# Kernel tuning notes

Hardware: AMD Instinct MI355X
Metric: run time of the kernel (lower is better)

## Reference

```python
import jax, jax.numpy as jnp
import numpy as np

B, C, H, W, KS = 8, 3, 512, 512, 3
K = KS * KS  # kernel_elements = 9


def setup_inputs() -> dict:
    key = jax.random.key(0)
    ks = jax.random.split(key, 5)
    return {
        "x": jax.random.normal(ks[0], (B, C, H, W), jnp.float32),
        "w1": jax.random.normal(ks[1], (K - 1, C, KS, KS), jnp.float32) * 0.1,  # find_ref conv weight
        "b1": jax.random.normal(ks[2], (K - 1,), jnp.float32) * 0.1,
        "w2": jax.random.normal(ks[3], (C, K), jnp.float32) * 0.1,  # grouped 1x1 conv: C groups, K in-ch each
        "b2": jax.random.normal(ks[4], (C,), jnp.float32) * 0.1,
    }


def _grid_sample_bilinear(img_nhwc, gx, gy):
    # torch.grid_sample, mode='bilinear', padding_mode='zeros', align_corners=False
    # img_nhwc: [B,H,W,C]; gx,gy: [B,h,w,K] normalized coords (x=width, y=height)
    Bs, Hh, Ww, _ = img_nhwc.shape
    ix = ((gx + 1.0) * Ww - 1.0) * 0.5
    iy = ((gy + 1.0) * Hh - 1.0) * 0.5
    ix0 = jnp.floor(ix)
    iy0 = jnp.floor(iy)
    wx1 = ix - ix0
    wy1 = iy - iy0
    wx0 = 1.0 - wx1
    wy0 = 1.0 - wy1
    bidx = jnp.arange(Bs)[:, None, None, None]

    def corner(yc, xc, wgt):
        valid = (xc >= 0) & (xc < Ww) & (yc >= 0) & (yc < Hh)
        xi = jnp.clip(xc, 0, Ww - 1).astype(jnp.int32)
        yi = jnp.clip(yc, 0, Hh - 1).astype(jnp.int32)
        v = img_nhwc[bidx, yi, xi]  # [B,h,w,K,C]
        return v * (wgt * valid)[..., None]

    out = corner(iy0, ix0, wy0 * wx0)
    out = out + corner(iy0, ix0 + 1.0, wy0 * wx1)
    out = out + corner(iy0 + 1.0, ix0, wy1 * wx0)
    out = out + corner(iy0 + 1.0, ix0 + 1.0, wy1 * wx1)
    return out  # [B,h,w,K,C]


def _forward(x, w1, b1, w2, b2):
    Bs, Cc, Hh, Ww = x.shape
    pad = KS // 2
    # find_ref: conv3x3 (pad=1) + sigmoid -> offsets in [0,1]
    off = jax.lax.conv_general_dilated(
        x, w1, (1, 1), ((pad, pad), (pad, pad)),
        dimension_numbers=("NCHW", "OIHW", "NCHW"))
    off = jax.nn.sigmoid(off + b1[None, :, None, None])  # [B,K-1,H,W]
    off = jnp.transpose(off, (0, 2, 3, 1)).reshape(Bs, Hh, Ww, (K - 1) // 2, 2)
    ctr = float(KS // 2)
    sym = 2.0 * ctr - off  # find_symmetric_points
    center = jnp.zeros((Bs, Hh, Ww, 1, 2), off.dtype)
    off_all = jnp.concatenate([off, center, sym], axis=-2)  # [B,H,W,K,2]
    # base grid: stack(h_grid, w_grid) with linspace(0,1)
    base = jnp.stack(
        jnp.meshgrid(jnp.linspace(0.0, 1.0, Hh), jnp.linspace(0.0, 1.0, Ww), indexing="ij"),
        axis=-1)  # [H,W,2]
    coords = base[None, :, :, None, :] + off_all  # [B,H,W,K,2]
    # grid_sample interprets last dim as (x=width, y=height)
    gx = coords[..., 0]
    gy = coords[..., 1]
    img = jnp.transpose(x, (0, 2, 3, 1))  # [B,H,W,C]
    sampled = _grid_sample_bilinear(img, gx, gy)  # [B,H,W,K,C]
    # concatenation order in torch: elem-major channels -> [B, K*C, H, W]
    deformed = jnp.transpose(sampled, (0, 3, 4, 1, 2)).reshape(Bs, K * Cc, Hh, Ww)
    # grouped 1x1 conv: groups=C, group g consumes channels [g*K:(g+1)*K]
    grp = deformed.reshape(Bs, Cc, K, Hh, Ww)
    out = jnp.einsum("bgkhw,gk->bghw", grp, w2) + b2[None, :, None, None]
    return jax.nn.relu(out)


def reference(x, w1, b1, w2, b2):
    return _forward(x, w1, b1, w2, b2)
```

## Files before the change

### kernel.cpp

```cpp
#include <hip/hip_runtime.h>

#define BATCH 8
#define HDIM  512
#define WDIM  512
#define PLANE (HDIM * WDIM)

#define QN      129
#define QPAIRS  (QN * QN)
#define QPLANE  (4 * QPAIRS * 8)
#define IMG12   (5 * QPLANE)

#define QC_N      129
#define YROW0     254
#define YROWS     259
#define YSTRIDE   260
#define QSTRIDE   (YSTRIDE * 16)
#define PARSTRIDE (QC_N * QSTRIDE)
#define IMGSTRIDE (2 * PARSTRIDE)

typedef _Float16 half2v __attribute__((ext_vector_type(2)));
typedef _Float16 half4v __attribute__((ext_vector_type(4)));
typedef _Float16 half8v __attribute__((ext_vector_type(8)));
typedef float    f2v    __attribute__((ext_vector_type(2)));

struct __align__(16) HQuad { half2v p0, p1, p2, p3; };
struct __align__(8)  HPair { half2v lo, hi; };

#if __has_builtin(__builtin_amdgcn_fdot2)
#define FDOT2(a, b, c) __builtin_amdgcn_fdot2((a), (b), (c), false)
#else
#define FDOT2(a, b, c) fmaf((float)(a).x, (float)(b).x, fmaf((float)(a).y, (float)(b).y, (c)))
#endif

#if __has_builtin(__builtin_amdgcn_exp2f)
#define EXP2F(x) __builtin_amdgcn_exp2f(x)
#else
#define EXP2F(x) exp2f(x)
#endif

__global__ __launch_bounds__(256) void repack_dots(
    const float* __restrict__ x,
    const float* __restrict__ w2,
    char* __restrict__ xp)
{
    int b  = blockIdx.x & 7;
    int P  = (blockIdx.x >> 3) & 3;
    int Qy = blockIdx.x >> 5;
    int Qx = threadIdx.x;
    if (Qx >= QN) return;
    int px = P & 1, py = P >> 1;
    int X0 = 2 * Qx + 254 + px;
    int Y0 = 2 * Qy + 254 + py;

    const float* xb = x + (size_t)b * 3 * PLANE;

    float vc[4][3];
#pragma unroll
    for (int cy = 0; cy < 2; cy++)
#pragma unroll
        for (int cx = 0; cx < 2; cx++) {
            int xx = X0 + cx, yy = Y0 + cy;
            bool vld = (xx <= 511) && (yy <= 511);
            int xs = min(xx, 511), ys = min(yy, 511);
            int base = (ys << 9) + xs;
            int ci = cy * 2 + cx;
            vc[ci][0] = vld ? xb[base]             : 0.f;
            vc[ci][1] = vld ? xb[PLANE + base]     : 0.f;
            vc[ci][2] = vld ? xb[2 * PLANE + base] : 0.f;
        }

    char* dst = xp + (size_t)b * IMG12 + (size_t)((P * QPAIRS + Qy * QN + Qx) << 3);
#pragma unroll
    for (int q = 0; q < 5; q++) {
        float wa = w2[3 * q], wb = w2[3 * q + 1], wc = w2[3 * q + 2];
        half4v o;
#pragma unroll
        for (int ci = 0; ci < 4; ci++) {
            float v = fmaf(vc[ci][2], wc, fmaf(vc[ci][1], wb, vc[ci][0] * wa));
            o[ci] = (_Float16)v;
        }
        *(half4v*)(dst + q * QPLANE) = o;
    }
}

__global__ __launch_bounds__(256) void seesaw_v12(
    const float* __restrict__ x,
    const char* __restrict__ xpack,
    const float* __restrict__ w1, const float* __restrict__ b1,
    const float* __restrict__ w2, const float* __restrict__ b2,
    float* __restrict__ out)
{
    int t  = threadIdx.x;
    int b  = blockIdx.x & 7;
    int i  = blockIdx.x >> 3;
    int j0 = t << 1;

    const float* xb = x + (size_t)b * 3 * PLANE;
    const char*  hb = xpack + (size_t)b * IMG12;

    int cm = j0 - 1; if (cm < 0) cm = 0;
    int cp = j0 + 2; if (cp > 511) cp = 511;
    bool jlo = (t == 0), jhi = (t == 255);

    float vm[9], va[9], vb9[9], vp9[9];
    if (i >= 1 && i <= 510) {
#pragma unroll
        for (int di = 0; di < 3; di++) {
            const float* row = xb + ((i + di - 1) << 9);
#pragma unroll
            for (int c = 0; c < 3; c++) {
                const float* rc = row + c * PLANE;
                float m = rc[cm]; if (jlo) m = 0.f;
                f2v  mid = *(const f2v*)(rc + j0);
                float pv = rc[cp]; if (jhi) pv = 0.f;
                int r = c * 3 + di;
                vm[r] = m; va[r] = mid[0]; vb9[r] = mid[1]; vp9[r] = pv;
            }
        }
    } else {
#pragma unroll
        for (int di = 0; di < 3; di++) {
            int y = i + di - 1;
            bool yv = (unsigned)y < (unsigned)HDIM;
            const float* row = xb + ((yv ? y : 0) << 9);
#pragma unroll
            for (int c = 0; c < 3; c++) {
                const float* rc = row + c * PLANE;
                float m = rc[cm]; if (jlo || !yv) m = 0.f;
                f2v  mid = *(const f2v*)(rc + j0);
                float pv = rc[cp]; if (jhi || !yv) pv = 0.f;
                float m0 = yv ? mid[0] : 0.f;
                float m1 = yv ? mid[1] : 0.f;
                int r = c * 3 + di;
                vm[r] = m; va[r] = m0; vb9[r] = m1; vp9[r] = pv;
            }
        }
    }
    __builtin_amdgcn_sched_barrier(0);

    float tap0[27], tap1[27];
#pragma unroll
    for (int c = 0; c < 3; c++)
#pragma unroll
        for (int di = 0; di < 3; di++) {
            int r = c * 3 + di, k = c * 9 + di * 3;
            tap0[k]     = vm[r];  tap0[k + 1] = va[r];  tap0[k + 2] = vb9[r];
            tap1[k]     = va[r];  tap1[k + 1] = vb9[r]; tap1[k + 2] = vp9[r];
        }

    const float NLOG2E = -1.44269504f;
    auto conv8 = [&](const float* tap, float* s2) {
        f2v V[13];
#pragma unroll
        for (int k = 0; k < 13; k++) { V[k][0] = tap[2 * k]; V[k][1] = tap[2 * k + 1]; }
#pragma unroll
        for (int e = 0; e < 8; e++) {
            const float* we = w1 + e * 27;
            f2v a2; a2[0] = b1[e]; a2[1] = 0.f;
#pragma unroll
            for (int k = 0; k < 13; k++) {
                f2v ww; ww[0] = we[2 * k]; ww[1] = we[2 * k + 1];
                a2 = __builtin_elementwise_fma(V[k], ww, a2);
            }
            float acc = a2[0] + a2[1] + tap[26] * we[26];
            s2[e] = 256.0f * __builtin_amdgcn_rcpf(1.0f + EXP2F(acc * NLOG2E));
        }
    };
    float s0[8], s1[8];
    conv8(tap0, s0);
    conv8(tap1, s1);

    const float k511 = 256.0f / 511.0f;
    float fxb = fmaf((float)i, k511, 255.5f);
    float fy0 = fmaf((float)j0, k511, 255.5f);
    float fy1 = fy0 + k511;

    int   adrA[5], adrB[5];
    float wXA[5][2], wYA[5][2], wXB[5][2], wYB[5][2];
    auto phase1 = [&](const float* s2, float fyb, int (&adr)[5],
                      float (&wX)[5][2], float (&wY)[5][2]) {
#pragma unroll
        for (int q = 0; q < 5; q++) {
            float ixf = (q < 4) ? (fxb + s2[2 * q])     : fxb;
            float iyf = (q < 4) ? (fyb + s2[2 * q + 1]) : fyb;
            int ix0 = (int)ixf, iy0 = (int)iyf;
            float wx1 = ixf - (float)ix0, wy1 = iyf - (float)iy0;
            wX[q][0] = (ix0 <= 511) ? (1.f - wx1) : 0.f;
            wX[q][1] = (ix0 <= 510) ? wx1 : 0.f;
            wY[q][0] = (iy0 <= 511) ? (1.f - wy1) : 0.f;
            wY[q][1] = (iy0 <= 510) ? wy1 : 0.f;
            int x0c = min(ix0, 511), y0c = min(iy0, 511);
            int P  = ((y0c & 1) << 1) | (x0c & 1);
            int Qx = (x0c >> 1) - 127;
            int Qy = (y0c >> 1) - 127;
            adr[q] = (P * QPAIRS + Qy * QN + Qx) << 3;
        }
    };

    phase1(s0, fy0, adrA, wXA, wYA);
    HPair pA[5];
#pragma unroll
    for (int q = 0; q < 5; q++)
        pA[q] = *(const HPair*)(hb + (size_t)(q * QPLANE + adrA[q]));
    phase1(s1, fy1, adrB, wXB, wYB);
    HPair pB[5];
#pragma unroll
    for (int q = 0; q < 5; q++)
        pB[q] = *(const HPair*)(hb + (size_t)(q * QPLANE + adrB[q]));
    __builtin_amdgcn_sched_barrier(0);

    float ogA[3] = {0.f, 0.f, 0.f}, ogB[3] = {0.f, 0.f, 0.f};
    auto phase3 = [&](HPair (&pv)[5], float (&wX)[5][2], float (&wY)[5][2], float* og) {
#pragma unroll
        for (int q = 0; q < 5; q++) {
            int g = q / 3;
            float v00 = (float)pv[q].lo[0], v01 = (float)pv[q].lo[1];
            float v10 = (float)pv[q].hi[0], v11c = (float)pv[q].hi[1];
            float r0 = fmaf(v01,  wX[q][1], v00 * wX[q][0]);
            float r1 = fmaf(v11c, wX[q][1], v10 * wX[q][0]);
            og[g] = fmaf(r1, wY[q][1], fmaf(r0, wY[q][0], og[g]));
        }
    };
    phase3(pA, wXA, wYA, ogA);
    phase3(pB, wXB, wYB, ogB);

    if ((i | j0) == 0) {
#pragma unroll
        for (int p = 5; p < 9; p++) {
            float ixf = fxb + 512.0f - s0[2 * (p - 5)];
            float iyf = fy0 + 512.0f - s0[2 * (p - 5) + 1];
            float ix0f = floorf(ixf), iy0f = floorf(iyf);
            float wx1 = ixf - ix0f, wy1 = iyf - iy0f;
            float wx0 = 1.f - wx1,  wy0 = 1.f - wy1;
            int ix0 = (int)ix0f, iy0 = (int)iy0f;
            float t0 = 0.f, t1 = 0.f, t2 = 0.f;
            for (int cy = 0; cy < 2; cy++) {
                int yc2 = iy0 + cy;
                if (yc2 < 0 || yc2 >= HDIM) continue;
                float wy = cy ? wy1 : wy0;
                for (int cx = 0; cx < 2; cx++) {
                    int xcc2 = ix0 + cx;
                    if (xcc2 < 0 || xcc2 >= WDIM) continue;
                    float wgt = wy * (cx ? wx1 : wx0);
                    int base = (yc2 << 9) + xcc2;
                    t0 = fmaf(xb[base],             wgt, t0);
                    t1 = fmaf(xb[PLANE + base],     wgt, t1);
                    t2 = fmaf(xb[2 * PLANE + base], wgt, t2);
                }
            }
            int g  = p / 3;
            int k0 = (p % 3) * 3;
            ogA[g] = fmaf(t0, w2[g * 9 + k0 + 0], ogA[g]);
            ogA[g] = fmaf(t1, w2[g * 9 + k0 + 1], ogA[g]);
            ogA[g] = fmaf(t2, w2[g * 9 + k0 + 2], ogA[g]);
        }
    }

    size_t ob = (size_t)(b * 3) * PLANE + ((size_t)i << 9) + j0;
#pragma unroll
    for (int g = 0; g < 3; g++) {
        float u0 = ogA[g] + b2[g];
        float u1 = ogB[g] + b2[g];
        f2v st;
        st[0] = u0 > 0.f ? u0 : 0.f;
        st[1] = u1 > 0.f ? u1 : 0.f;
        *(f2v*)(out + ob + (size_t)g * PLANE) = st;
    }
}

__global__ __launch_bounds__(256) void repack_tiles(
    const float* __restrict__ x, char* __restrict__ xp)
{
    int b    = blockIdx.x & 7;
    int rest = blockIdx.x >> 3;
    int p    = rest & 1;
    int Qc   = rest >> 1;
    int xb0  = 254 + 2 * Qc + p;
    int x1   = xb0 + 1;
    bool x1v = (x1 < 512);

    const float* xb = x + (size_t)b * 3 * PLANE;
    char* dst = xp + (size_t)b * IMGSTRIDE + (size_t)p * PARSTRIDE
                   + (size_t)Qc * QSTRIDE;

    for (int t = threadIdx.x; t < YROWS; t += 256) {
        int y = YROW0 + t;
        half8v o;
        if (y < 512) {
            int base = (y << 9) + xb0;
            float a0 = xb[base];
            float a1 = xb[PLANE + base];
            float a2 = xb[2 * PLANE + base];
            float b0 = 0.f, b1c = 0.f, b2c = 0.f;
            if (x1v) {
                b0  = xb[base + 1];
                b1c = xb[PLANE + base + 1];
                b2c = xb[2 * PLANE + base + 1];
            }
            o[0] = (_Float16)a0; o[1] = (_Float16)a1; o[2] = (_Float16)a2; o[3] = (_Float16)0.f;
            o[4] = (_Float16)b0; o[5] = (_Float16)b1c; o[6] = (_Float16)b2c; o[7] = (_Float16)0.f;
        } else {
#pragma unroll
            for (int k = 0; k < 8; k++) o[k] = (_Float16)0.f;
        }
        *(half8v*)(dst + (size_t)t * 16) = o;
    }
}

__global__ __launch_bounds__(256) void seesaw_v11(
    const float* __restrict__ x, const char* __restrict__ xpack,
    const float* __restrict__ w1, const float* __restrict__ b1,
    const float* __restrict__ w2, const float* __restrict__ b2,
    float* __restrict__ out)
{
    int t  = threadIdx.x;
    int b  = blockIdx.x & 7;
    int i  = blockIdx.x >> 3;
    int j0 = t << 1;

    const float* xb = x + (size_t)b * 3 * PLANE;
    const char*  hb = xpack + (size_t)b * IMGSTRIDE;

    int cm = j0 - 1; if (cm < 0) cm = 0;
    int cp = j0 + 2; if (cp > 511) cp = 511;
    bool jlo = (t == 0), jhi = (t == 255);

    float vm[9], va[9], vb9[9], vp9[9];
    if (i >= 1 && i <= 510) {
#pragma unroll
        for (int di = 0; di < 3; di++) {
            const float* row = xb + ((i + di - 1) << 9);
#pragma unroll
            for (int c = 0; c < 3; c++) {
                const float* rc = row + c * PLANE;
                float m = rc[cm]; if (jlo) m = 0.f;
                f2v  mid = *(const f2v*)(rc + j0);
                float pv = rc[cp]; if (jhi) pv = 0.f;
                int r = c * 3 + di;
                vm[r] = m; va[r] = mid[0]; vb9[r] = mid[1]; vp9[r] = pv;
            }
        }
    } else {
#pragma unroll
        for (int di = 0; di < 3; di++) {
            int y = i + di - 1;
            bool yv = (unsigned)y < (unsigned)HDIM;
            const float* row = xb + ((yv ? y : 0) << 9);
#pragma unroll
            for (int c = 0; c < 3; c++) {
                const float* rc = row + c * PLANE;
                float m = rc[cm]; if (jlo || !yv) m = 0.f;
                f2v  mid = *(const f2v*)(rc + j0);
                float pv = rc[cp]; if (jhi || !yv) pv = 0.f;
                float m0 = yv ? mid[0] : 0.f;
                float m1 = yv ? mid[1] : 0.f;
                int r = c * 3 + di;
                vm[r] = m; va[r] = m0; vb9[r] = m1; vp9[r] = pv;
            }
        }
    }
    __builtin_amdgcn_sched_barrier(0);

    float tap0[27], tap1[27];
#pragma unroll
    for (int c = 0; c < 3; c++)
#pragma unroll
        for (int di = 0; di < 3; di++) {
            int r = c * 3 + di, k = c * 9 + di * 3;
            tap0[k]     = vm[r];  tap0[k + 1] = va[r];  tap0[k + 2] = vb9[r];
            tap1[k]     = va[r];  tap1[k + 1] = vb9[r]; tap1[k + 2] = vp9[r];
        }

    const float NLOG2E = -1.44269504f;
    auto conv8 = [&](const float* tap, float* s2) {
        f2v V[13];
#pragma unroll
        for (int k = 0; k < 13; k++) { V[k][0] = tap[2 * k]; V[k][1] = tap[2 * k + 1]; }
#pragma unroll
        for (int e = 0; e < 8; e++) {
            const float* we = w1 + e * 27;
            f2v a2; a2[0] = b1[e]; a2[1] = 0.f;
#pragma unroll
            for (int k = 0; k < 13; k++) {
                f2v ww; ww[0] = we[2 * k]; ww[1] = we[2 * k + 1];
                a2 = __builtin_elementwise_fma(V[k], ww, a2);
            }
            float acc = a2[0] + a2[1] + tap[26] * we[26];
            s2[e] = 256.0f * __builtin_amdgcn_rcpf(1.0f + EXP2F(acc * NLOG2E));
        }
    };
    float s0[8], s1[8];
    conv8(tap0, s0);
    conv8(tap1, s1);

    half2v w2a[5], w2b[5];
#pragma unroll
    for (int q = 0; q < 5; q++) {
        w2a[q][0] = (_Float16)w2[q * 3];
        w2a[q][1] = (_Float16)w2[q * 3 + 1];
        w2b[q][0] = (_Float16)w2[q * 3 + 2];
        w2b[q][1] = (_Float16)0.f;
    }

    const float k511 = 256.0f / 511.0f;
    float fxb = fmaf((float)i, k511, 255.5f);
    float fy0 = fmaf((float)j0, k511, 255.5f);
    float fy1 = fy0 + k511;

    int   adrA[5], adrB[5];
    float wXA[5][2], wYA[5][2], wXB[5][2], wYB[5][2];
    auto phase1 = [&](const float* s2, float fyb, int (&adr)[5],
                      float (&wX)[5][2], float (&wY)[5][2]) {
#pragma unroll
        for (int q = 0; q < 5; q++) {
            float ixf = (q < 4) ? (fxb + s2[2 * q])     : fxb;
            float iyf = (q < 4) ? (fyb + s2[2 * q + 1]) : fyb;
            int ix0 = (int)ixf, iy0 = (int)iyf;
            float wx1 = ixf - (float)ix0, wy1 = iyf - (float)iy0;
            wX[q][0] = (ix0 <= 511) ? (1.f - wx1) : 0.f;
            wX[q][1] = (ix0 <= 510) ? wx1 : 0.f;
            wY[q][0] = (iy0 <= 511) ? (1.f - wy1) : 0.f;
            wY[q][1] = (iy0 <= 510) ? wy1 : 0.f;
            int x0c = min(ix0, 511);
            int y0c = min(iy0, 511);
            int Qc  = (x0c >> 1) - 127;
            int off = (Qc << 12) + (Qc << 6) + ((y0c - 254) << 4);
            adr[q] = off + ((x0c & 1) ? PARSTRIDE : 0);
        }
    };

    phase1(s0, fy0, adrA, wXA, wYA);
    HQuad qA[5][2];
#pragma unroll
    for (int q = 0; q < 5; q++) {
        qA[q][0] = *(const HQuad*)(hb + (size_t)adrA[q]);
        qA[q][1] = *(const HQuad*)(hb + (size_t)adrA[q] + 16);
    }
    phase1(s1, fy1, adrB, wXB, wYB);
    HQuad qB[5][2];
#pragma unroll
    for (int q = 0; q < 5; q++) {
        qB[q][0] = *(const HQuad*)(hb + (size_t)adrB[q]);
        qB[q][1] = *(const HQuad*)(hb + (size_t)adrB[q] + 16);
    }
    __builtin_amdgcn_sched_barrier(0);

    float ogA[3] = {0.f, 0.f, 0.f}, ogB[3] = {0.f, 0.f, 0.f};
    auto phase3 = [&](HQuad (&qv)[5][2], float (&wX)[5][2], float (&wY)[5][2], float* og) {
#pragma unroll
        for (int q = 0; q < 5; q++) {
            int g = q / 3;
            float dl0 = FDOT2(qv[q][0].p0, w2a[q], FDOT2(qv[q][0].p1, w2b[q], 0.f));
            float dh0 = FDOT2(qv[q][0].p2, w2a[q], FDOT2(qv[q][0].p3, w2b[q], 0.f));
            float dl1 = FDOT2(qv[q][1].p0, w2a[q], FDOT2(qv[q][1].p1, w2b[q], 0.f));
            float dh1 = FDOT2(qv[q][1].p2, w2a[q], FDOT2(qv[q][1].p3, w2b[q], 0.f));
            float r0 = fmaf(dh0, wX[q][1], dl0 * wX[q][0]);
            float r1 = fmaf(dh1, wX[q][1], dl1 * wX[q][0]);
            og[g] = fmaf(r1, wY[q][1], fmaf(r0, wY[q][0], og[g]));
        }
    };
    phase3(qA, wXA, wYA, ogA);
    phase3(qB, wXB, wYB, ogB);

    if ((i | j0) == 0) {
#pragma unroll
        for (int p = 5; p < 9; p++) {
            float ixf = fxb + 512.0f - s0[2 * (p - 5)];
            float iyf = fy0 + 512.0f - s0[2 * (p - 5) + 1];
            float ix0f = floorf(ixf), iy0f = floorf(iyf);
            float wx1 = ixf - ix0f, wy1 = iyf - iy0f;
            float wx0 = 1.f - wx1,  wy0 = 1.f - wy1;
            int ix0 = (int)ix0f, iy0 = (int)iy0f;
            float t0 = 0.f, t1 = 0.f, t2 = 0.f;
            for (int cy = 0; cy < 2; cy++) {
                int yc2 = iy0 + cy;
                if (yc2 < 0 || yc2 >= HDIM) continue;
                float wy = cy ? wy1 : wy0;
                for (int cx = 0; cx < 2; cx++) {
                    int xcc2 = ix0 + cx;
                    if (xcc2 < 0 || xcc2 >= WDIM) continue;
                    float wgt = wy * (cx ? wx1 : wx0);
                    int base = (yc2 << 9) + xcc2;
                    t0 = fmaf(xb[base],             wgt, t0);
                    t1 = fmaf(xb[PLANE + base],     wgt, t1);
                    t2 = fmaf(xb[2 * PLANE + base], wgt, t2);
                }
            }
            int g  = p / 3;
            int k0 = (p % 3) * 3;
            ogA[g] = fmaf(t0, w2[g * 9 + k0 + 0], ogA[g]);
            ogA[g] = fmaf(t1, w2[g * 9 + k0 + 1], ogA[g]);
            ogA[g] = fmaf(t2, w2[g * 9 + k0 + 2], ogA[g]);
        }
    }

    size_t ob = (size_t)(b * 3) * PLANE + ((size_t)i << 9) + j0;
#pragma unroll
    for (int g = 0; g < 3; g++) {
        float u0 = ogA[g] + b2[g];
        float u1 = ogB[g] + b2[g];
        f2v st;
        st[0] = u0 > 0.f ? u0 : 0.f;
        st[1] = u1 > 0.f ? u1 : 0.f;
        *(f2v*)(out + ob + (size_t)g * PLANE) = st;
    }
}

__global__ __launch_bounds__(256) void seesaw_fused_v1(
    const float* __restrict__ x, const float* __restrict__ w1,
    const float* __restrict__ b1, const float* __restrict__ w2,
    const float* __restrict__ b2, float* __restrict__ out)
{
    int t = threadIdx.x;
    int gid = blockIdx.x * 256 + t;
    int j = gid & (WDIM - 1);
    int i = (gid >> 9) & (HDIM - 1);
    int b = gid >> 18;
    const float* xb = x + (size_t)b * 3 * PLANE;
    float acc[8];
#pragma unroll
    for (int e = 0; e < 8; e++) acc[e] = b1[e];
#pragma unroll
    for (int di = 0; di < 3; di++) {
        int y = i + di - 1;
        if (y < 0 || y >= HDIM) continue;
#pragma unroll
        for (int dj = 0; dj < 3; dj++) {
            int xc = j + dj - 1;
            if (xc < 0 || xc >= WDIM) continue;
            size_t base = (size_t)y * WDIM + xc;
#pragma unroll
            for (int c = 0; c < 3; c++) {
                float v = xb[(size_t)c * PLANE + base];
#pragma unroll
                for (int e = 0; e < 8; e++)
                    acc[e] = fmaf(v, w1[e * 27 + c * 9 + di * 3 + dj], acc[e]);
            }
        }
    }
    float s[8];
#pragma unroll
    for (int e = 0; e < 8; e++) s[e] = 1.0f / (1.0f + __expf(-acc[e]));
    const float inv511 = 1.0f / 511.0f;
    float bx = (float)i * inv511, by = (float)j * inv511;
    float og0 = 0.f, og1 = 0.f, og2 = 0.f;
#pragma unroll
    for (int p = 0; p < 9; p++) {
        float c0, c1;
        if (p < 4)       { c0 = s[2 * p];              c1 = s[2 * p + 1]; }
        else if (p == 4) { c0 = 0.f;                   c1 = 0.f; }
        else             { c0 = 2.0f - s[2 * (p - 5)]; c1 = 2.0f - s[2 * (p - 5) + 1]; }
        float ixf = (bx + c0) * 256.0f + 255.5f;
        float iyf = (by + c1) * 256.0f + 255.5f;
        float ix0f = floorf(ixf), iy0f = floorf(iyf);
        float wx1 = ixf - ix0f, wy1 = iyf - iy0f;
        float wx0 = 1.f - wx1,  wy0 = 1.f - wy1;
        int ix0 = (int)ix0f, iy0 = (int)iy0f;
        float s0 = 0.f, s1 = 0.f, s2 = 0.f;
#pragma unroll
        for (int cy = 0; cy < 2; cy++) {
            int yc = iy0 + cy;
            if (yc < 0 || yc >= HDIM) continue;
            float wy = cy ? wy1 : wy0;
#pragma unroll
            for (int cx = 0; cx < 2; cx++) {
                int xcc = ix0 + cx;
                if (xcc < 0 || xcc >= WDIM) continue;
                float wgt = wy * (cx ? wx1 : wx0);
                size_t base = (size_t)yc * WDIM + xcc;
                s0 = fmaf(xb[base],             wgt, s0);
                s1 = fmaf(xb[PLANE + base],     wgt, s1);
                s2 = fmaf(xb[2 * PLANE + base], wgt, s2);
            }
        }
        int g  = p / 3;
        int k0 = (p % 3) * 3;
        float* og = (g == 0) ? &og0 : (g == 1) ? &og1 : &og2;
        *og = fmaf(s0, w2[g * 9 + k0 + 0], *og);
        *og = fmaf(s1, w2[g * 9 + k0 + 1], *og);
        *og = fmaf(s2, w2[g * 9 + k0 + 2], *og);
    }
    size_t ob = (size_t)(b * 3) * PLANE + (size_t)i * WDIM + j;
    float v0 = og0 + b2[0], v1 = og1 + b2[1], v2 = og2 + b2[2];
    out[ob]             = v0 > 0.f ? v0 : 0.f;
    out[ob + PLANE]     = v1 > 0.f ? v1 : 0.f;
    out[ob + 2 * PLANE] = v2 > 0.f ? v2 : 0.f;
}

extern "C" void kernel_launch(void* const* d_in, const int* in_sizes, int n_in,
                              void* d_out, int out_size, void* d_ws, size_t ws_size,
                              hipStream_t stream) {
    const float* x  = (const float*)d_in[0];
    const float* w1 = (const float*)d_in[1];
    const float* b1 = (const float*)d_in[2];
    const float* w2 = (const float*)d_in[3];
    const float* b2 = (const float*)d_in[4];
    float* out = (float*)d_out;

    int total = BATCH * HDIM * WDIM;
    size_t need12 = (size_t)BATCH * IMG12 + 64;
    size_t need11 = (size_t)BATCH * IMGSTRIDE + 16;

    if (ws_size >= need12) {
        repack_dots<<<8 * 4 * QN, 256, 0, stream>>>(x, w2, (char*)d_ws);
        seesaw_v12<<<BATCH * HDIM, 256, 0, stream>>>(x, (const char*)d_ws,
                                                     w1, b1, w2, b2, out);
    } else if (ws_size >= need11) {
        repack_tiles<<<8 * 2 * QC_N, 256, 0, stream>>>(x, (char*)d_ws);
        seesaw_v11<<<BATCH * HDIM, 256, 0, stream>>>(x, (const char*)d_ws,
                                                     w1, b1, w2, b2, out);
    } else {
        seesaw_fused_v1<<<total / 256, 256, 0, stream>>>(x, w1, b1, w2, b2, out);
    }
}
```

Measured before the change: 120.5 us.

## Compute one pixel per thread and prepack transposed conv weights for vector FMA

The main kernel now gives each thread a single output pixel instead of two adjacent ones, which doubles the grid and lowers the register footprint per thread. The repack kernel also writes w1 in a transposed layout into the workspace, so the 27x8 offset conv can run as packed float2 FMAs over pairs of output channels. The seesaw_v11 and repack_tiles fallback is reordered in the file, not changed. In exchange, adjacent pixels no longer share their conv tap loads, so there is more redundant global and cache traffic, and the weights are read from global memory rather than as uniform scalars.

Result: no change. 121.1 us (+0.5%).

```diff
diff --git a/kernel.cpp b/kernel.cpp
--- a/kernel.cpp
+++ b/kernel.cpp
@@ -9,6 +9,8 @@
 #define QPAIRS  (QN * QN)
 #define QPLANE  (4 * QPAIRS * 8)
 #define IMG12   (5 * QPLANE)
+#define PACKBYTES ((size_t)BATCH * IMG12)
+#define W1E_FLOATS (27 * 8)
 
 #define QC_N      129
 #define YROW0     254
@@ -40,9 +42,16 @@
 
 __global__ __launch_bounds__(256) void repack_dots(
     const float* __restrict__ x,
+    const float* __restrict__ w1,
     const float* __restrict__ w2,
     char* __restrict__ xp)
 {
+    if (blockIdx.x == 0 && threadIdx.x < W1E_FLOATS) {
+        int t = threadIdx.x;
+        float* w1e = (float*)(xp + PACKBYTES);
+        w1e[t] = w1[(t & 7) * 27 + (t >> 3)];
+    }
+
     int b  = blockIdx.x & 7;
     int P  = (blockIdx.x >> 3) & 3;
     int Qy = blockIdx.x >> 5;
@@ -83,9 +92,203 @@
     }
 }
 
-__global__ __launch_bounds__(256) void seesaw_v12(
+__global__ __launch_bounds__(256) void seesaw_v13(
     const float* __restrict__ x,
     const char* __restrict__ xpack,
+    const float* __restrict__ b1,
+    const float* __restrict__ w2, const float* __restrict__ b2,
+    float* __restrict__ out)
+{
+    int t    = threadIdx.x;
+    int b    = blockIdx.x & 7;
+    int rest = blockIdx.x >> 3;
+    int i    = rest >> 1;
+    int j    = ((rest & 1) << 8) + t;
+
+    const float* xb = x + (size_t)b * 3 * PLANE;
+    const char*  hb = xpack + (size_t)b * IMG12;
+    const f2v*   wv = (const f2v*)(xpack + PACKBYTES);
+
+    float tap[27];
+    int cm1 = j - 1; if (cm1 < 0) cm1 = 0;
+    int cp1 = j + 1; if (cp1 > 511) cp1 = 511;
+    bool jlo = (j == 0), jhi = (j == 511);
+
+    if (i >= 1 && i <= 510) {
+#pragma unroll
+        for (int di = 0; di < 3; di++) {
+            const float* row = xb + ((i + di - 1) << 9);
+#pragma unroll
+            for (int c = 0; c < 3; c++) {
+                const float* rc = row + c * PLANE;
+                float vm = rc[cm1]; if (jlo) vm = 0.f;
+                float v0 = rc[j];
+                float vp = rc[cp1]; if (jhi) vp = 0.f;
+                tap[c * 9 + di * 3 + 0] = vm;
+                tap[c * 9 + di * 3 + 1] = v0;
+                tap[c * 9 + di * 3 + 2] = vp;
+            }
+        }
+    } else {
+#pragma unroll
+        for (int di = 0; di < 3; di++) {
+            int y = i + di - 1;
+            bool yv = (unsigned)y < (unsigned)HDIM;
+            const float* row = xb + ((yv ? y : 0) << 9);
+#pragma unroll
+            for (int c = 0; c < 3; c++) {
+                const float* rc = row + c * PLANE;
+                float vm = rc[cm1]; if (jlo || !yv) vm = 0.f;
+                float v0 = rc[j];   if (!yv)        v0 = 0.f;
+                float vp = rc[cp1]; if (jhi || !yv) vp = 0.f;
+                tap[c * 9 + di * 3 + 0] = vm;
+                tap[c * 9 + di * 3 + 1] = v0;
+                tap[c * 9 + di * 3 + 2] = vp;
+            }
+        }
+    }
+    __builtin_amdgcn_sched_barrier(0);
+
+    f2v acc2[4];
+#pragma unroll
+    for (int eh = 0; eh < 4; eh++) { acc2[eh][0] = b1[2 * eh]; acc2[eh][1] = b1[2 * eh + 1]; }
+#pragma unroll
+    for (int k = 0; k < 27; k++) {
+        f2v tk; tk[0] = tap[k]; tk[1] = tap[k];
+#pragma unroll
+        for (int eh = 0; eh < 4; eh++)
+            acc2[eh] = __builtin_elementwise_fma(tk, wv[k * 4 + eh], acc2[eh]);
+    }
+
+    const float NLOG2E = -1.44269504f;
+    float s256[8];
+#pragma unroll
+    for (int e = 0; e < 8; e++) {
+        float acc = acc2[e >> 1][e & 1];
+        s256[e] = 256.0f * __builtin_amdgcn_rcpf(1.0f + EXP2F(acc * NLOG2E));
+    }
+
+    const float k511 = 256.0f / 511.0f;
+    float fxb = fmaf((float)i, k511, 255.5f);
+    float fyb = fmaf((float)j, k511, 255.5f);
+
+    int   adr[5];
+    float wX[5][2], wY[5][2];
+#pragma unroll
+    for (int q = 0; q < 5; q++) {
+        float ixf = (q < 4) ? (fxb + s256[2 * q])     : fxb;
+        float iyf = (q < 4) ? (fyb + s256[2 * q + 1]) : fyb;
+        int ix0 = (int)ixf, iy0 = (int)iyf;
+        float wx1 = ixf - (float)ix0, wy1 = iyf - (float)iy0;
+        wX[q][0] = (ix0 <= 511) ? (1.f - wx1) : 0.f;
+        wX[q][1] = (ix0 <= 510) ? wx1 : 0.f;
+        wY[q][0] = (iy0 <= 511) ? (1.f - wy1) : 0.f;
+        wY[q][1] = (iy0 <= 510) ? wy1 : 0.f;
+        int x0c = min(ix0, 511), y0c = min(iy0, 511);
+        int P  = ((y0c & 1) << 1) | (x0c & 1);
+        int Qx = (x0c >> 1) - 127;
+        int Qy = (y0c >> 1) - 127;
+        adr[q] = (P * QPAIRS + Qy * QN + Qx) << 3;
+    }
+
+    HPair pv[5];
+#pragma unroll
+    for (int q = 0; q < 5; q++)
+        pv[q] = *(const HPair*)(hb + (size_t)(q * QPLANE + adr[q]));
+    __builtin_amdgcn_sched_barrier(0);
+
+    float og[3] = {0.f, 0.f, 0.f};
+#pragma unroll
+    for (int q = 0; q < 5; q++) {
+        int g = q / 3;
+        float v00 = (float)pv[q].lo[0], v01 = (float)pv[q].lo[1];
+        float v10 = (float)pv[q].hi[0], v11c = (float)pv[q].hi[1];
+        float r0 = fmaf(v01,  wX[q][1], v00 * wX[q][0]);
+        float r1 = fmaf(v11c, wX[q][1], v10 * wX[q][0]);
+        og[g] = fmaf(r1, wY[q][1], fmaf(r0, wY[q][0], og[g]));
+    }
+
+    if ((i | j) == 0) {
+#pragma unroll
+        for (int p = 5; p < 9; p++) {
+            float ixf = fxb + 512.0f - s256[2 * (p - 5)];
+            float iyf = fyb + 512.0f - s256[2 * (p - 5) + 1];
+            float ix0f = floorf(ixf), iy0f = floorf(iyf);
+            float wx1 = ixf - ix0f, wy1 = iyf - iy0f;
+            float wx0 = 1.f - wx1,  wy0 = 1.f - wy1;
+            int ix0 = (int)ix0f, iy0 = (int)iy0f;
+            float t0 = 0.f, t1 = 0.f, t2 = 0.f;
+            for (int cy = 0; cy < 2; cy++) {
+                int yc2 = iy0 + cy;
+                if (yc2 < 0 || yc2 >= HDIM) continue;
+                float wy = cy ? wy1 : wy0;
+                for (int cx = 0; cx < 2; cx++) {
+                    int xcc2 = ix0 + cx;
+                    if (xcc2 < 0 || xcc2 >= WDIM) continue;
+                    float wgt = wy * (cx ? wx1 : wx0);
+                    int base = (yc2 << 9) + xcc2;
+                    t0 = fmaf(xb[base],             wgt, t0);
+                    t1 = fmaf(xb[PLANE + base],     wgt, t1);
+                    t2 = fmaf(xb[2 * PLANE + base], wgt, t2);
+                }
+            }
+            int g  = p / 3;
+            int k0 = (p % 3) * 3;
+            og[g] = fmaf(t0, w2[g * 9 + k0 + 0], og[g]);
+            og[g] = fmaf(t1, w2[g * 9 + k0 + 1], og[g]);
+            og[g] = fmaf(t2, w2[g * 9 + k0 + 2], og[g]);
+        }
+    }
+
+    size_t ob = (size_t)(b * 3) * PLANE + ((size_t)i << 9) + j;
+#pragma unroll
+    for (int g = 0; g < 3; g++) {
+        float vv = og[g] + b2[g];
+        out[ob + (size_t)g * PLANE] = vv > 0.f ? vv : 0.f;
+    }
+}
+
+__global__ __launch_bounds__(256) void repack_tiles(
+    const float* __restrict__ x, char* __restrict__ xp)
+{
+    int b    = blockIdx.x & 7;
+    int rest = blockIdx.x >> 3;
+    int p    = rest & 1;
+    int Qc   = rest >> 1;
+    int xb0  = 254 + 2 * Qc + p;
+    int x1   = xb0 + 1;
+    bool x1v = (x1 < 512);
+
+    const float* xb = x + (size_t)b * 3 * PLANE;
+    char* dst = xp + (size_t)b * IMGSTRIDE + (size_t)p * PARSTRIDE
+                   + (size_t)Qc * QSTRIDE;
+
+    for (int t = threadIdx.x; t < YROWS; t += 256) {
+        int y = YROW0 + t;
+        half8v o;
+        if (y < 512) {
+            int base = (y << 9) + xb0;
+            float a0 = xb[base];
+            float a1 = xb[PLANE + base];
+            float a2 = xb[2 * PLANE + base];
+            float b0 = 0.f, b1c = 0.f, b2c = 0.f;
+            if (x1v) {
+                b0  = xb[base + 1];
+                b1c = xb[PLANE + base + 1];
+                b2c = xb[2 * PLANE + base + 1];
+            }
+            o[0] = (_Float16)a0; o[1] = (_Float16)a1; o[2] = (_Float16)a2; o[3] = (_Float16)0.f;
+            o[4] = (_Float16)b0; o[5] = (_Float16)b1c; o[6] = (_Float16)b2c; o[7] = (_Float16)0.f;
+        } else {
+#pragma unroll
+            for (int k = 0; k < 8; k++) o[k] = (_Float16)0.f;
+        }
+        *(half8v*)(dst + (size_t)t * 16) = o;
+    }
+}
+
+__global__ __launch_bounds__(256) void seesaw_v11(
+    const float* __restrict__ x, const char* __restrict__ xpack,
     const float* __restrict__ w1, const float* __restrict__ b1,
     const float* __restrict__ w2, const float* __restrict__ b2,
     float* __restrict__ out)
@@ -96,7 +299,7 @@
     int j0 = t << 1;
 
     const float* xb = x + (size_t)b * 3 * PLANE;
-    const char*  hb = xpack + (size_t)b * IMG12;
+    const char*  hb = xpack + (size_t)b * IMGSTRIDE;
 
     int cm = j0 - 1; if (cm < 0) cm = 0;
     int cp = j0 + 2; if (cp > 511) cp = 511;
@@ -170,6 +373,15 @@
     conv8(tap0, s0);
     conv8(tap1, s1);
 
+    half2v w2a[5], w2b[5];
+#pragma unroll
+    for (int q = 0; q < 5; q++) {
+        w2a[q][0] = (_Float16)w2[q * 3];
+        w2a[q][1] = (_Float16)w2[q * 3 + 1];
+        w2b[q][0] = (_Float16)w2[q * 3 + 2];
+        w2b[q][1] = (_Float16)0.f;
+    }
+
     const float k511 = 256.0f / 511.0f;
     float fxb = fmaf((float)i, k511, 255.5f);
     float fy0 = fmaf((float)j0, k511, 255.5f);
@@ -189,40 +401,46 @@
             wX[q][1] = (ix0 <= 510) ? wx1 : 0.f;
             wY[q][0] = (iy0 <= 511) ? (1.f - wy1) : 0.f;
             wY[q][1] = (iy0 <= 510) ? wy1 : 0.f;
-            int x0c = min(ix0, 511), y0c = min(iy0, 511);
-            int P  = ((y0c & 1) << 1) | (x0c & 1);
-            int Qx = (x0c >> 1) - 127;
-            int Qy = (y0c >> 1) - 127;
-            adr[q] = (P * QPAIRS + Qy * QN + Qx) << 3;
+            int x0c = min(ix0, 511);
+            int y0c = min(iy0, 511);
+            int Qc  = (x0c >> 1) - 127;
+            int off = (Qc << 12) + (Qc << 6) + ((y0c - 254) << 4);
+            adr[q] = off + ((x0c & 1) ? PARSTRIDE : 0);
         }
     };
 
     phase1(s0, fy0, adrA, wXA, wYA);
-    HPair pA[5];
-#pragma unroll
-    for (int q = 0; q < 5; q++)
-        pA[q] = *(const HPair*)(hb + (size_t)(q * QPLANE + adrA[q]));
+    HQuad qA[5][2];
+#pragma unroll
+    for (int q = 0; q < 5; q++) {
+        qA[q][0] = *(const HQuad*)(hb + (size_t)adrA[q]);
+        qA[q][1] = *(const HQuad*)(hb + (size_t)adrA[q] + 16);
+    }
     phase1(s1, fy1, adrB, wXB, wYB);
-    HPair pB[5];
-#pragma unroll
-    for (int q = 0; q < 5; q++)
-        pB[q] = *(const HPair*)(hb + (size_t)(q * QPLANE + adrB[q]));
+    HQuad qB[5][2];
+#pragma unroll
+    for (int q = 0; q < 5; q++) {
+        qB[q][0] = *(const HQuad*)(hb + (size_t)adrB[q]);
+        qB[q][1] = *(const HQuad*)(hb + (size_t)adrB[q] + 16);
+    }
     __builtin_amdgcn_sched_barrier(0);
 
     float ogA[3] = {0.f, 0.f, 0.f}, ogB[3] = {0.f, 0.f, 0.f};
-    auto phase3 = [&](HPair (&pv)[5], float (&wX)[5][2], float (&wY)[5][2], float* og) {
+    auto phase3 = [&](HQuad (&qv)[5][2], float (&wX)[5][2], float (&wY)[5][2], float* og) {
 #pragma unroll
         for (int q = 0; q < 5; q++) {
             int g = q / 3;
-            float v00 = (float)pv[q].lo[0], v01 = (float)pv[q].lo[1];
-            float v10 = (float)pv[q].hi[0], v11c = (float)pv[q].hi[1];
-            float r0 = fmaf(v01,  wX[q][1], v00 * wX[q][0]);
-            float r1 = fmaf(v11c, wX[q][1], v10 * wX[q][0]);
+            float dl0 = FDOT2(qv[q][0].p0, w2a[q], FDOT2(qv[q][0].p1, w2b[q], 0.f));
+            float dh0 = FDOT2(qv[q][0].p2, w2a[q], FDOT2(qv[q][0].p3, w2b[q], 0.f));
+            float dl1 = FDOT2(qv[q][1].p0, w2a[q], FDOT2(qv[q][1].p1, w2b[q], 0.f));
+            float dh1 = FDOT2(qv[q][1].p2, w2a[q], FDOT2(qv[q][1].p3, w2b[q], 0.f));
+            float r0 = fmaf(dh0, wX[q][1], dl0 * wX[q][0]);
+            float r1 = fmaf(dh1, wX[q][1], dl1 * wX[q][0]);
             og[g] = fmaf(r1, wY[q][1], fmaf(r0, wY[q][0], og[g]));
         }
     };
-    phase3(pA, wXA, wYA, ogA);
-    phase3(pB, wXB, wYB, ogB);
+    phase3(qA, wXA, wYA, ogA);
+    phase3(qB, wXB, wYB, ogB);
 
     if ((i | j0) == 0) {
 #pragma unroll
@@ -268,244 +486,6 @@
     }
 }
 
-__global__ __launch_bounds__(256) void repack_tiles(
-    const float* __restrict__ x, char* __restrict__ xp)
-{
-    int b    = blockIdx.x & 7;
-    int rest = blockIdx.x >> 3;
-    int p    = rest & 1;
-    int Qc   = rest >> 1;
-    int xb0  = 254 + 2 * Qc + p;
-    int x1   = xb0 + 1;
-    bool x1v = (x1 < 512);
-
-    const float* xb = x + (size_t)b * 3 * PLANE;
-    char* dst = xp + (size_t)b * IMGSTRIDE + (size_t)p * PARSTRIDE
-                   + (size_t)Qc * QSTRIDE;
-
-    for (int t = threadIdx.x; t < YROWS; t += 256) {
-        int y = YROW0 + t;
-        half8v o;
-        if (y < 512) {
-            int base = (y << 9) + xb0;
-            float a0 = xb[base];
-            float a1 = xb[PLANE + base];
-            float a2 = xb[2 * PLANE + base];
-            float b0 = 0.f, b1c = 0.f, b2c = 0.f;
-            if (x1v) {
-                b0  = xb[base + 1];
-                b1c = xb[PLANE + base + 1];
-                b2c = xb[2 * PLANE + base + 1];
-            }
-            o[0] = (_Float16)a0; o[1] = (_Float16)a1; o[2] = (_Float16)a2; o[3] = (_Float16)0.f;
-            o[4] = (_Float16)b0; o[5] = (_Float16)b1c; o[6] = (_Float16)b2c; o[7] = (_Float16)0.f;
-        } else {
-#pragma unroll
-            for (int k = 0; k < 8; k++) o[k] = (_Float16)0.f;
-        }
-        *(half8v*)(dst + (size_t)t * 16) = o;
-    }
-}
-
-__global__ __launch_bounds__(256) void seesaw_v11(
-    const float* __restrict__ x, const char* __restrict__ xpack,
-    const float* __restrict__ w1, const float* __restrict__ b1,
-    const float* __restrict__ w2, const float* __restrict__ b2,
-    float* __restrict__ out)
-{
-    int t  = threadIdx.x;
-    int b  = blockIdx.x & 7;
-    int i  = blockIdx.x >> 3;
-    int j0 = t << 1;
-
-    const float* xb = x + (size_t)b * 3 * PLANE;
-    const char*  hb = xpack + (size_t)b * IMGSTRIDE;
-
-    int cm = j0 - 1; if (cm < 0) cm = 0;
-    int cp = j0 + 2; if (cp > 511) cp = 511;
-    bool jlo = (t == 0), jhi = (t == 255);
-
-    float vm[9], va[9], vb9[9], vp9[9];
-    if (i >= 1 && i <= 510) {
-#pragma unroll
-        for (int di = 0; di < 3; di++) {
-            const float* row = xb + ((i + di - 1) << 9);
-#pragma unroll
-            for (int c = 0; c < 3; c++) {
-                const float* rc = row + c * PLANE;
-                float m = rc[cm]; if (jlo) m = 0.f;
-                f2v  mid = *(const f2v*)(rc + j0);
-                float pv = rc[cp]; if (jhi) pv = 0.f;
-                int r = c * 3 + di;
-                vm[r] = m; va[r] = mid[0]; vb9[r] = mid[1]; vp9[r] = pv;
-            }
-        }
-    } else {
-#pragma unroll
-        for (int di = 0; di < 3; di++) {
-            int y = i + di - 1;
-            bool yv = (unsigned)y < (unsigned)HDIM;
-            const float* row = xb + ((yv ? y : 0) << 9);
-#pragma unroll
-            for (int c = 0; c < 3; c++) {
-                const float* rc = row + c * PLANE;
-                float m = rc[cm]; if (jlo || !yv) m = 0.f;
-                f2v  mid = *(const f2v*)(rc + j0);
-                float pv = rc[cp]; if (jhi || !yv) pv = 0.f;
-                float m0 = yv ? mid[0] : 0.f;
-                float m1 = yv ? mid[1] : 0.f;
-                int r = c * 3 + di;
-                vm[r] = m; va[r] = m0; vb9[r] = m1; vp9[r] = pv;
-            }
-        }
-    }
-    __builtin_amdgcn_sched_barrier(0);
-
-    float tap0[27], tap1[27];
-#pragma unroll
-    for (int c = 0; c < 3; c++)
-#pragma unroll
-        for (int di = 0; di < 3; di++) {
-            int r = c * 3 + di, k = c * 9 + di * 3;
-            tap0[k]     = vm[r];  tap0[k + 1] = va[r];  tap0[k + 2] = vb9[r];
-            tap1[k]     = va[r];  tap1[k + 1] = vb9[r]; tap1[k + 2] = vp9[r];
-        }
-
-    const float NLOG2E = -1.44269504f;
-    auto conv8 = [&](const float* tap, float* s2) {
-        f2v V[13];
-#pragma unroll
-        for (int k = 0; k < 13; k++) { V[k][0] = tap[2 * k]; V[k][1] = tap[2 * k + 1]; }
-#pragma unroll
-        for (int e = 0; e < 8; e++) {
-            const float* we = w1 + e * 27;
-            f2v a2; a2[0] = b1[e]; a2[1] = 0.f;
-#pragma unroll
-            for (int k = 0; k < 13; k++) {
-                f2v ww; ww[0] = we[2 * k]; ww[1] = we[2 * k + 1];
-                a2 = __builtin_elementwise_fma(V[k], ww, a2);
-            }
-            float acc = a2[0] + a2[1] + tap[26] * we[26];
-            s2[e] = 256.0f * __builtin_amdgcn_rcpf(1.0f + EXP2F(acc * NLOG2E));
-        }
-    };
-    float s0[8], s1[8];
-    conv8(tap0, s0);
-    conv8(tap1, s1);
-
-    half2v w2a[5], w2b[5];
-#pragma unroll
-    for (int q = 0; q < 5; q++) {
-        w2a[q][0] = (_Float16)w2[q * 3];
-        w2a[q][1] = (_Float16)w2[q * 3 + 1];
-        w2b[q][0] = (_Float16)w2[q * 3 + 2];
-        w2b[q][1] = (_Float16)0.f;
-    }
-
-    const float k511 = 256.0f / 511.0f;
-    float fxb = fmaf((float)i, k511, 255.5f);
-    float fy0 = fmaf((float)j0, k511, 255.5f);
-    float fy1 = fy0 + k511;
-
-    int   adrA[5], adrB[5];
-    float wXA[5][2], wYA[5][2], wXB[5][2], wYB[5][2];
-    auto phase1 = [&](const float* s2, float fyb, int (&adr)[5],
-                      float (&wX)[5][2], float (&wY)[5][2]) {
-#pragma unroll
-        for (int q = 0; q < 5; q++) {
-            float ixf = (q < 4) ? (fxb + s2[2 * q])     : fxb;
-            float iyf = (q < 4) ? (fyb + s2[2 * q + 1]) : fyb;
-            int ix0 = (int)ixf, iy0 = (int)iyf;
-            float wx1 = ixf - (float)ix0, wy1 = iyf - (float)iy0;
-            wX[q][0] = (ix0 <= 511) ? (1.f - wx1) : 0.f;
-            wX[q][1] = (ix0 <= 510) ? wx1 : 0.f;
-            wY[q][0] = (iy0 <= 511) ? (1.f - wy1) : 0.f;
-            wY[q][1] = (iy0 <= 510) ? wy1 : 0.f;
-            int x0c = min(ix0, 511);
-            int y0c = min(iy0, 511);
-            int Qc  = (x0c >> 1) - 127;
-            int off = (Qc << 12) + (Qc << 6) + ((y0c - 254) << 4);
-            adr[q] = off + ((x0c & 1) ? PARSTRIDE : 0);
-        }
-    };
-
-    phase1(s0, fy0, adrA, wXA, wYA);
-    HQuad qA[5][2];
-#pragma unroll
-    for (int q = 0; q < 5; q++) {
-        qA[q][0] = *(const HQuad*)(hb + (size_t)adrA[q]);
-        qA[q][1] = *(const HQuad*)(hb + (size_t)adrA[q] + 16);
-    }
-    phase1(s1, fy1, adrB, wXB, wYB);
-    HQuad qB[5][2];
-#pragma unroll
-    for (int q = 0; q < 5; q++) {
-        qB[q][0] = *(const HQuad*)(hb + (size_t)adrB[q]);
-        qB[q][1] = *(const HQuad*)(hb + (size_t)adrB[q] + 16);
-    }
-    __builtin_amdgcn_sched_barrier(0);
-
-    float ogA[3] = {0.f, 0.f, 0.f}, ogB[3] = {0.f, 0.f, 0.f};
-    auto phase3 = [&](HQuad (&qv)[5][2], float (&wX)[5][2], float (&wY)[5][2], float* og) {
-#pragma unroll
-        for (int q = 0; q < 5; q++) {
-            int g = q / 3;
-            float dl0 = FDOT2(qv[q][0].p0, w2a[q], FDOT2(qv[q][0].p1, w2b[q], 0.f));
-            float dh0 = FDOT2(qv[q][0].p2, w2a[q], FDOT2(qv[q][0].p3, w2b[q], 0.f));
-            float dl1 = FDOT2(qv[q][1].p0, w2a[q], FDOT2(qv[q][1].p1, w2b[q], 0.f));
-            float dh1 = FDOT2(qv[q][1].p2, w2a[q], FDOT2(qv[q][1].p3, w2b[q], 0.f));
-            float r0 = fmaf(dh0, wX[q][1], dl0 * wX[q][0]);
-            float r1 = fmaf(dh1, wX[q][1], dl1 * wX[q][0]);
-            og[g] = fmaf(r1, wY[q][1], fmaf(r0, wY[q][0], og[g]));
-        }
-    };
-    phase3(qA, wXA, wYA, ogA);
-    phase3(qB, wXB, wYB, ogB);
-
-    if ((i | j0) == 0) {
-#pragma unroll
-        for (int p = 5; p < 9; p++) {
-            float ixf = fxb + 512.0f - s0[2 * (p - 5)];
-            float iyf = fy0 + 512.0f - s0[2 * (p - 5) + 1];
-            float ix0f = floorf(ixf), iy0f = floorf(iyf);
-            float wx1 = ixf - ix0f, wy1 = iyf - iy0f;
-            float wx0 = 1.f - wx1,  wy0 = 1.f - wy1;
-            int ix0 = (int)ix0f, iy0 = (int)iy0f;
-            float t0 = 0.f, t1 = 0.f, t2 = 0.f;
-            for (int cy = 0; cy < 2; cy++) {
-                int yc2 = iy0 + cy;
-                if (yc2 < 0 || yc2 >= HDIM) continue;
-                float wy = cy ? wy1 : wy0;
-                for (int cx = 0; cx < 2; cx++) {
-                    int xcc2 = ix0 + cx;
-                    if (xcc2 < 0 || xcc2 >= WDIM) continue;
-                    float wgt = wy * (cx ? wx1 : wx0);
-                    int base = (yc2 << 9) + xcc2;
-                    t0 = fmaf(xb[base],             wgt, t0);
-                    t1 = fmaf(xb[PLANE + base],     wgt, t1);
-                    t2 = fmaf(xb[2 * PLANE + base], wgt, t2);
-                }
-            }
-            int g  = p / 3;
-            int k0 = (p % 3) * 3;
-            ogA[g] = fmaf(t0, w2[g * 9 + k0 + 0], ogA[g]);
-            ogA[g] = fmaf(t1, w2[g * 9 + k0 + 1], ogA[g]);
-            ogA[g] = fmaf(t2, w2[g * 9 + k0 + 2], ogA[g]);
-        }
-    }
-
-    size_t ob = (size_t)(b * 3) * PLANE + ((size_t)i << 9) + j0;
-#pragma unroll
-    for (int g = 0; g < 3; g++) {
-        float u0 = ogA[g] + b2[g];
-        float u1 = ogB[g] + b2[g];
-        f2v st;
-        st[0] = u0 > 0.f ? u0 : 0.f;
-        st[1] = u1 > 0.f ? u1 : 0.f;
-        *(f2v*)(out + ob + (size_t)g * PLANE) = st;
-    }
-}
-
 __global__ __launch_bounds__(256) void seesaw_fused_v1(
     const float* __restrict__ x, const float* __restrict__ w1,
     const float* __restrict__ b1, const float* __restrict__ w2,
@@ -598,13 +578,13 @@
     float* out = (float*)d_out;
 
     int total = BATCH * HDIM * WDIM;
-    size_t need12 = (size_t)BATCH * IMG12 + 64;
+    size_t need13 = PACKBYTES + W1E_FLOATS * 4 + 64;
     size_t need11 = (size_t)BATCH * IMGSTRIDE + 16;
 
-    if (ws_size >= need12) {
-        repack_dots<<<8 * 4 * QN, 256, 0, stream>>>(x, w2, (char*)d_ws);
-        seesaw_v12<<<BATCH * HDIM, 256, 0, stream>>>(x, (const char*)d_ws,
-                                                     w1, b1, w2, b2, out);
+    if (ws_size >= need13) {
+        repack_dots<<<8 * 4 * QN, 256, 0, stream>>>(x, w1, w2, (char*)d_ws);
+        seesaw_v13<<<total / 256, 256, 0, stream>>>(x, (const char*)d_ws,
+                                                    b1, w2, b2, out);
     } else if (ws_size >= need11) {
         repack_tiles<<<8 * 2 * QC_N, 256, 0, stream>>>(x, (char*)d_ws);
         seesaw_v11<<<BATCH * HDIM, 256, 0, stream>>>(x, (const char*)d_ws,
```
